# Optimization experiments

Hardware: AMD Instinct MI355X
Metric: run time of the kernel (lower is better)

## Reference

```python
import jax, jax.numpy as jnp
import numpy as np
import math

DIM = 256; SEQ = 2048; BSZ = 32; NI = 128; NS = 4; ITERS = 3

def _ln(x, g, b):
    m = x.mean(-1, keepdims=True)
    v = ((x - m) ** 2).mean(-1, keepdims=True)
    return (x - m) / jnp.sqrt(v + 1e-5) * g + b

def _norm(x):
    # torch F.normalize: x / ||x||.clamp_min(1e-12)
    return x / jnp.clip(jnp.linalg.norm(x, axis=-1, keepdims=True), 1e-12, None)

def setup_inputs() -> dict:
    key = jax.random.key(0)
    ks = jax.random.split(key, 16)
    def w(k, shape, s=0.02):
        return jax.random.normal(k, shape, jnp.float32) * s
    return {
        'tokens': jax.random.normal(ks[0], (BSZ, SEQ, DIM), jnp.float32),
        'cls_embed': jax.random.normal(ks[1], (BSZ, DIM), jnp.float32),
        'intent_queries': jax.random.normal(ks[2], (NI, DIM), jnp.float32),
        'noise': jax.random.normal(ks[3], (NI, BSZ, NS, DIM), jnp.float32),
        'Wk': w(ks[4], (DIM, DIM)), 'bk': jnp.zeros(DIM, jnp.float32),
        'Wv': w(ks[5], (DIM, DIM)), 'bv': jnp.zeros(DIM, jnp.float32),
        'Wqs': w(ks[6], (DIM, DIM)), 'bqs': jnp.zeros(DIM, jnp.float32),
        'Wqi': w(ks[7], (DIM, DIM)), 'bqi': jnp.zeros(DIM, jnp.float32),
        'ln1_g': jnp.ones(DIM, jnp.float32), 'ln1_b': jnp.zeros(DIM, jnp.float32),
        'ln2_g': jnp.ones(DIM, jnp.float32), 'ln2_b': jnp.zeros(DIM, jnp.float32),
        'Wf1': w(ks[8], (DIM, 2 * DIM)), 'bf1': jnp.zeros(2 * DIM, jnp.float32),
        'Wf2': w(ks[9], (2 * DIM, DIM)), 'bf2': jnp.zeros(DIM, jnp.float32),
        'slot_mu': w(ks[10], (1, NS, DIM)),  # randn*0.02
        'slot_sigma': jnp.ones((1, NS, DIM), jnp.float32) * 0.1,
        'alpha': jnp.float32(1.0),
        'temperature': jnp.float32(1.0),
    }

def reference(tokens, cls_embed, intent_queries, noise, Wk, bk, Wv, bv,
              Wqs, bqs, Wqi, bqi, ln1_g, ln1_b, ln2_g, ln2_b,
              Wf1, bf1, Wf2, bf2, slot_mu, slot_sigma, alpha, temperature):
    scale = 1.0 / math.sqrt(DIM)
    # k/v are identical across the per-intent loop in the original -> compute once
    k = tokens @ Wk + bk  # [B,S,D]
    v = tokens @ Wv + bv  # [B,S,D]
    cls_n = _norm(cls_embed)  # [B,D]

    def per_intent(q, eps):  # q: [D], eps: [B,NS,D]
        qn = _norm(q)
        q_intent = (q @ Wqi + bqi)[None, None, :]  # broadcast over [B,NS,:]
        slots = slot_mu[0] + eps * slot_sigma[0]   # [B,NS,D]
        for _ in range(ITERS):
            q_slot = slots @ Wqs + bqs + q_intent
            logit = jnp.einsum('bnd,bsd->bns', q_slot, k) * scale
            attn = jax.nn.softmax(logit, axis=-1)
            upd = jnp.einsum('bns,bsd->bnd', attn, v)
            slots = _ln(slots + upd, ln1_g, ln1_b)
            h = _ln(slots, ln2_g, ln2_b)
            slots = slots + jax.nn.gelu(h @ Wf1 + bf1, approximate=False) @ Wf2 + bf2
        sn = _norm(slots)                               # [B,NS,D]
        a = jax.nn.softmax(jnp.einsum('bnd,d->bn', sn, qn), axis=-1)
        summ = jnp.einsum('bn,bnd->bd', a, slots)       # slot_summary
        fused = cls_n + alpha * _norm(summ)
        return fused @ qn                               # [B]

    scores = jax.vmap(per_intent)(intent_queries, noise)  # [NI,B]
    logits = scores.T / jnp.maximum(temperature, 1e-4)    # [B,NI]
    return logits
```

## Files before the change

### kernel.cpp

```cpp
#include <hip/hip_runtime.h>
#include <math.h>

#define BSZ 32
#define NI  128

typedef __attribute__((ext_vector_type(8))) _Float16 f16x8;
typedef __attribute__((ext_vector_type(4))) _Float16 f16x4;
typedef __attribute__((ext_vector_type(4))) float    f32x4;

#define MFMA16(a, b, c) __builtin_amdgcn_mfma_f32_16x16x32_f16((a), (b), (c), 0, 0, 0)

#define GLL(g, l) __builtin_amdgcn_global_load_lds(                          \
    (const __attribute__((address_space(1))) void*)(g),                      \
    (__attribute__((address_space(3))) void*)(l), 16, 0, 0)

#define LGKM_BAR() do {                                                      \
    asm volatile("s_waitcnt lgkmcnt(0)" ::: "memory");                       \
    __builtin_amdgcn_sched_barrier(0);                                       \
    __builtin_amdgcn_s_barrier();                                            \
    __builtin_amdgcn_sched_barrier(0); } while (0)

__device__ inline float dot4f(float4 a, float4 b) {
    return a.x * b.x + a.y * b.y + a.z * b.z + a.w * b.w;
}

__device__ inline float4* slp(float* base, int r, int c) {
    return (float4*)(base + r * 256 + ((((c) >> 2) ^ (r & 7)) << 2));
}

__device__ inline void tpose64(const float* __restrict__ src, int Csrc,
                               _Float16* __restrict__ dstT, int KT,
                               int r0, int c0, _Float16 (*tbuf)[72], int tid)
{
#pragma unroll
    for (int it = 0; it < 4; it++) {
        int idx = tid + it * 256;
        int rr = idx >> 4, c4 = idx & 15;
        float4 w = *(const float4*)(src + (size_t)(r0 + rr) * Csrc + c0 + c4 * 4);
        tbuf[c4 * 4 + 0][rr] = (_Float16)w.x;
        tbuf[c4 * 4 + 1][rr] = (_Float16)w.y;
        tbuf[c4 * 4 + 2][rr] = (_Float16)w.z;
        tbuf[c4 * 4 + 3][rr] = (_Float16)w.w;
    }
    __syncthreads();
#pragma unroll
    for (int it = 0; it < 2; it++) {
        int idx = tid + it * 256;
        int orr = idx >> 3, oc8 = idx & 7;
        int n = c0 + orr;
        size_t tile = (size_t)(n >> 4) * KT + (r0 >> 5) + (oc8 >> 2);
        *(f16x8*)(dstT + tile * 512 + (n & 15) * 32 + (oc8 & 3) * 8) = *(const f16x8*)&tbuf[orr][oc8 * 8];
    }
}

__global__ __launch_bounds__(256) void prep(
    const float* __restrict__ Wk, const float* __restrict__ Wv,
    const float* __restrict__ Wqs, const float* __restrict__ Wf1,
    const float* __restrict__ Wf2,
    const float* __restrict__ intent_q, const float* __restrict__ Wqi,
    const float* __restrict__ bqi, const float* __restrict__ bqs,
    const float* __restrict__ cls_embed,
    _Float16* __restrict__ wkT, _Float16* __restrict__ wvT,
    _Float16* __restrict__ wqsT, _Float16* __restrict__ wf1T,
    _Float16* __restrict__ wf2T,
    float* __restrict__ qint2, float* __restrict__ qn, float* __restrict__ clsn)
{
    __shared__ _Float16 tbuf[64][72];
    __shared__ float buf[256];
    __shared__ float red[4];
    const int t = threadIdx.x, blk = blockIdx.x;
    const int lane = t & 63, w = t >> 6;

    if (blk < 112) {
        if (blk < 16)       tpose64(Wk, 256, wkT, 8, (blk >> 2) * 64, (blk & 3) * 64, tbuf, t);
        else if (blk < 32)  { int tt = blk - 16; tpose64(Wv, 256, wvT, 8, (tt >> 2) * 64, (tt & 3) * 64, tbuf, t); }
        else if (blk < 48)  { int tt = blk - 32; tpose64(Wqs, 256, wqsT, 8, (tt >> 2) * 64, (tt & 3) * 64, tbuf, t); }
        else if (blk < 80)  { int tt = blk - 48; tpose64(Wf1, 512, wf1T, 8, (tt & 3) * 64, (tt >> 2) * 64, tbuf, t); }
        else                { int tt = blk - 80; tpose64(Wf2, 256, wf2T, 16, (tt >> 2) * 64, (tt & 3) * 64, tbuf, t); }
    } else if (blk < 240) {
        int i = blk - 112;
        float x = intent_q[(size_t)i * 256 + t];
        buf[t] = x;
        float ss = x * x;
#pragma unroll
        for (int m = 1; m < 64; m <<= 1) ss += __shfl_xor(ss, m, 64);
        if (lane == 0) red[w] = ss;
        __syncthreads();
        float tot = red[0] + red[1] + red[2] + red[3];
        qn[(size_t)i * 256 + t] = x / fmaxf(sqrtf(tot), 1e-12f);
        float acc = bqi[t] + bqs[t];
        for (int e = 0; e < 256; e += 4) {
            const float4 q4 = *(const float4*)&buf[e];
            acc += q4.x * Wqi[(size_t)(e + 0) * 256 + t];
            acc += q4.y * Wqi[(size_t)(e + 1) * 256 + t];
            acc += q4.z * Wqi[(size_t)(e + 2) * 256 + t];
            acc += q4.w * Wqi[(size_t)(e + 3) * 256 + t];
        }
        qint2[(size_t)i * 256 + t] = acc;
    } else {
        int b = blk - 240;
        float x = cls_embed[(size_t)b * 256 + t];
        float ss = x * x;
#pragma unroll
        for (int m = 1; m < 64; m <<= 1) ss += __shfl_xor(ss, m, 64);
        if (lane == 0) red[w] = ss;
        __syncthreads();
        float tot = red[0] + red[1] + red[2] + red[3];
        clsn[(size_t)b * 256 + t] = x / fmaxf(sqrtf(tot), 1e-12f);
    }
}

__global__ __launch_bounds__(512, 2) void kvf_k(
    const float* __restrict__ tokens,
    const _Float16* __restrict__ wkT, const _Float16* __restrict__ wvT,
    const float* __restrict__ bk, const float* __restrict__ bv,
    _Float16* __restrict__ kT, _Float16* __restrict__ vT)
{
    __shared__ __align__(16) _Float16 Sb[2][8192];

    const int t = threadIdx.x, lane = t & 63, w = t >> 6;
    const int l15 = lane & 15, quad = lane >> 4;
    const int lofs = l15 * 32 + quad * 8;
    const int bx = blockIdx.x;
    const int b = bx & 31, chunk = bx >> 5;

    f16x8 wk[2][8], wv[2][8];
#pragma unroll
    for (int j = 0; j < 2; j++)
#pragma unroll
        for (int ks = 0; ks < 8; ks++) {
            wk[j][ks] = *(const f16x8*)(wkT + ((size_t)(2 * w + j) * 8 + ks) * 512 + lofs);
            wv[j][ks] = *(const f16x8*)(wvT + ((size_t)(2 * w + j) * 8 + ks) * 512 + lofs);
        }
    f32x4 bi0 = *(const f32x4*)(bk + w * 32 + quad * 4);
    f32x4 bi1 = *(const f32x4*)(bk + w * 32 + 16 + quad * 4);
    const float bv0 = bv[(2 * w) * 16 + l15];
    const float bv1 = bv[(2 * w + 1) * 16 + l15];

    const int rr = t >> 5, d8 = t & 31;
    const float* tbase = tokens + ((size_t)b * 2048 + chunk * 256) * 256 + rr * 256 + d8 * 8;
    const int wofs0 = (d8 >> 2) * 512 + rr * 32 + (d8 & 3) * 8;
    const int wofs1 = (8 + (d8 >> 2)) * 512 + rr * 32 + (d8 & 3) * 8;

    float4 pa0, pa1, pb0, pb1;

#define KVF_LOADS(P) do {                                                    \
        const float* sp_ = tbase + (size_t)(P) * 8192;                       \
        pa0 = *(const float4*)(sp_);                                         \
        pa1 = *(const float4*)(sp_ + 4);                                     \
        pb0 = *(const float4*)(sp_ + 4096);                                  \
        pb1 = *(const float4*)(sp_ + 4100);                                  \
    } while (0)

#define KVF_STAGE(BUF) do {                                                  \
        f16x8 h0, h1;                                                        \
        h0[0] = (_Float16)pa0.x; h0[1] = (_Float16)pa0.y;                    \
        h0[2] = (_Float16)pa0.z; h0[3] = (_Float16)pa0.w;                    \
        h0[4] = (_Float16)pa1.x; h0[5] = (_Float16)pa1.y;                    \
        h0[6] = (_Float16)pa1.z; h0[7] = (_Float16)pa1.w;                    \
        h1[0] = (_Float16)pb0.x; h1[1] = (_Float16)pb0.y;                    \
        h1[2] = (_Float16)pb0.z; h1[3] = (_Float16)pb0.w;                    \
        h1[4] = (_Float16)pb1.x; h1[5] = (_Float16)pb1.y;                    \
        h1[6] = (_Float16)pb1.z; h1[7] = (_Float16)pb1.w;                    \
        *(f16x8*)((BUF) + wofs0) = h0;                                       \
        *(f16x8*)((BUF) + wofs1) = h1;                                       \
    } while (0)

    KVF_LOADS(0);
    KVF_STAGE(&Sb[0][0]);
    LGKM_BAR();

    for (int p = 0; p < 8; p++) {
        if (p < 7) KVF_LOADS(p + 1);
        __builtin_amdgcn_sched_barrier(0);

        const _Float16* lb = &Sb[p & 1][0];
        const int stg0 = chunk * 16 + p * 2;
        const int sp = chunk * 8 + p;

        f16x8 a[2][8];
#pragma unroll
        for (int st = 0; st < 2; st++)
#pragma unroll
            for (int ks = 0; ks < 8; ks++)
                a[st][ks] = *(const f16x8*)(lb + (st * 8 + ks) * 512 + lofs);

#pragma unroll
        for (int st = 0; st < 2; st++) {
            f32x4 c0 = {0.f, 0.f, 0.f, 0.f}, c1 = {0.f, 0.f, 0.f, 0.f};
#pragma unroll
            for (int ks = 0; ks < 8; ks++) {
                c0 = MFMA16(wk[0][ks], a[st][ks], c0);
                c1 = MFMA16(wk[1][ks], a[st][ks], c1);
            }
            f16x4 p0, p1;
#pragma unroll
            for (int reg = 0; reg < 4; reg++) {
                p0[reg] = (_Float16)(c0[reg] + bi0[reg]);
                p1[reg] = (_Float16)(c1[reg] + bi1[reg]);
            }
            _Float16* tp = kT + ((size_t)(b * 128 + stg0 + st) * 8 + w) * 512 + l15 * 32;
            *(f16x4*)(tp + (quad >> 1) * 8 + (quad & 1) * 4) = p0;
            *(f16x4*)(tp + (2 + (quad >> 1)) * 8 + (quad & 1) * 4) = p1;
        }

#pragma unroll
        for (int j = 0; j < 2; j++) {
            f32x4 c0 = {0.f, 0.f, 0.f, 0.f}, c1 = {0.f, 0.f, 0.f, 0.f};
#pragma unroll
            for (int ks = 0; ks < 8; ks++) {
                c0 = MFMA16(a[0][ks], wv[j][ks], c0);
                c1 = MFMA16(a[1][ks], wv[j][ks], c1);
            }
            const float bb = j ? bv1 : bv0;
            f16x4 p0, p1;
#pragma unroll
            for (int reg = 0; reg < 4; reg++) {
                p0[reg] = (_Float16)(c0[reg] + bb);
                p1[reg] = (_Float16)(c1[reg] + bb);
            }
            _Float16* tp = vT + ((size_t)(b * 16 + 2 * w + j) * 64 + sp) * 512 + l15 * 32;
            *(f16x4*)(tp + (quad >> 1) * 8 + (quad & 1) * 4) = p0;
            *(f16x4*)(tp + (2 + (quad >> 1)) * 8 + (quad & 1) * 4) = p1;
        }

        if (p < 7) {
            KVF_STAGE(&Sb[(p + 1) & 1][0]);
            LGKM_BAR();
        }
    }
#undef KVF_LOADS
#undef KVF_STAGE
}

__global__ __launch_bounds__(256) void slots_init(
    const float* __restrict__ noise, const float* __restrict__ slot_mu,
    const float* __restrict__ slot_sigma, float* __restrict__ slots,
    _Float16* __restrict__ slotsT)
{
    int idx = blockIdx.x * 256 + threadIdx.x;
    int row = idx >> 5, d8 = idx & 31;
    int b = row >> 9, i = (row >> 2) & 127, n = row & 3;
    int d = d8 * 8;
    const float* mp = slot_mu + n * 256 + d;
    const float* sp = slot_sigma + n * 256 + d;
    const float* np = noise + (((size_t)i * BSZ + b) * 4 + n) * 256 + d;
    float4 o0, o1;
    {
        float4 mu = *(const float4*)mp, sg = *(const float4*)sp, ns = *(const float4*)np;
        o0.x = mu.x + ns.x * sg.x; o0.y = mu.y + ns.y * sg.y;
        o0.z = mu.z + ns.z * sg.z; o0.w = mu.w + ns.w * sg.w;
    }
    {
        float4 mu = *(const float4*)(mp + 4), sg = *(const float4*)(sp + 4), ns = *(const float4*)(np + 4);
        o1.x = mu.x + ns.x * sg.x; o1.y = mu.y + ns.y * sg.y;
        o1.z = mu.z + ns.z * sg.z; o1.w = mu.w + ns.w * sg.w;
    }
    *(float4*)(slots + (size_t)row * 256 + d) = o0;
    *(float4*)(slots + (size_t)row * 256 + d + 4) = o1;
    f16x8 h;
    h[0] = (_Float16)o0.x; h[1] = (_Float16)o0.y; h[2] = (_Float16)o0.z; h[3] = (_Float16)o0.w;
    h[4] = (_Float16)o1.x; h[5] = (_Float16)o1.y; h[6] = (_Float16)o1.z; h[7] = (_Float16)o1.w;
    *(f16x8*)(slotsT + ((size_t)(row >> 4) * 8 + (d8 >> 2)) * 512 + (row & 15) * 32 + (d8 & 3) * 8) = h;
}

__global__ __launch_bounds__(256) void qslot_k(
    const _Float16* __restrict__ slotsT, const _Float16* __restrict__ wqsT,
    const float* __restrict__ qint2, _Float16* __restrict__ qsT)
{
    const int tid = threadIdx.x, lane = tid & 63, wv = tid >> 6;
    const int l15 = lane & 15, quad = lane >> 4;
    const int lofs = l15 * 32 + quad * 8;
    const int bx = blockIdx.x, rb = bx >> 2, dq = bx & 3;
    const int rt = rb * 4 + wv;
    const int gr0 = rt * 16;

    f16x8 bs[8];
#pragma unroll
    for (int ks = 0; ks < 8; ks++)
        bs[ks] = *(const f16x8*)(slotsT + ((size_t)rt * 8 + ks) * 512 + lofs);
    const int iq = ((gr0 + l15) & 511) >> 2;
#pragma unroll
    for (int dt = 0; dt < 4; dt++) {
        int dti = dq * 4 + dt;
        f32x4 c = {0.f, 0.f, 0.f, 0.f};
#pragma unroll
        for (int ks = 0; ks < 8; ks++)
            c = MFMA16(*(const f16x8*)(wqsT + ((size_t)dti * 8 + ks) * 512 + lofs), bs[ks], c);
        float4 qi = *(const float4*)(qint2 + (size_t)iq * 256 + dti * 16 + quad * 4);
        f16x4 o;
#pragma unroll
        for (int reg = 0; reg < 4; reg++) o[reg] = (_Float16)((c[reg] + qi[reg]) * 0.0625f);
        *(f16x4*)(qsT + ((size_t)rt * 8 + (dti >> 1)) * 512 + l15 * 32
                  + ((dti & 1) * 2 + (quad >> 1)) * 8 + (quad & 1) * 4) = o;
    }
}

__global__ __launch_bounds__(512, 2) void attn_k(
    const _Float16* __restrict__ qsT, const _Float16* __restrict__ kT,
    const _Float16* __restrict__ vT,
    _Float16* __restrict__ Opart, float* __restrict__ psum4)
{
    __shared__ __align__(16) _Float16 Kb[2][16384];
    __shared__ __align__(16) _Float16 Vb[16384];
    __shared__ __align__(16) _Float16 pb[8][2304];

    const int tid = threadIdx.x, lane = tid & 63, wv = tid >> 6;
    const int l15 = lane & 15, quad = lane >> 4;
    const int lofs = l15 * 32 + quad * 8;
    const int bx = blockIdx.x;
    const int b = bx & 31, rb = (bx >> 5) & 1, sk = bx >> 6;
    const int gr0 = b * 512 + rb * 256 + wv * 32;
    const int rt_q = gr0 >> 4;

    _Float16* pw = pb[wv];

    const _Float16* kSrc = kT + ((size_t)(b * 128 + sk * 32) * 8) * 512;

    {
        const _Float16* src = kSrc + (size_t)(wv * 4) * 512 + lane * 8;
        _Float16* dst = &Kb[0][(wv * 4) * 512 + lane * 8];
#pragma unroll
        for (int j = 0; j < 4; j++) GLL(src + j * 512, dst + j * 512);
    }

    f16x8 q[2][8];
#pragma unroll
    for (int m = 0; m < 2; m++)
#pragma unroll
        for (int ks = 0; ks < 8; ks++)
            q[m][ks] = *(const f16x8*)(qsT + ((size_t)(rt_q + m) * 8 + ks) * 512 + lofs);

    f32x4 O[2][16];
#pragma unroll
    for (int m = 0; m < 2; m++)
#pragma unroll
        for (int dt = 0; dt < 16; dt++) O[m][dt] = (f32x4){0.f, 0.f, 0.f, 0.f};
    float ps[2][4] = {{0.f, 0.f, 0.f, 0.f}, {0.f, 0.f, 0.f, 0.f}};

    asm volatile("s_waitcnt vmcnt(0)" ::: "memory");
    __builtin_amdgcn_s_barrier();
    __builtin_amdgcn_sched_barrier(0);

    for (int s = 0; s < 8; s++) {
        const int cur = s & 1;

        {
            const int seg0 = wv * 4;
#pragma unroll
            for (int j = 0; j < 4; j++) {
                const int seg = seg0 + j;
                const _Float16* src = vT
                    + ((size_t)(b * 16 + (seg >> 1)) * 64 + sk * 16 + s * 2 + (seg & 1)) * 512
                    + lane * 8;
                GLL(src, &Vb[seg * 512 + lane * 8]);
            }
        }
        if (s < 7) {
            const _Float16* src = kSrc + (size_t)(s + 1) * 16384 + (wv * 4) * 512 + lane * 8;
            _Float16* dst = &Kb[cur ^ 1][(wv * 4) * 512 + lane * 8];
#pragma unroll
            for (int j = 0; j < 4; j++) GLL(src + j * 512, dst + j * 512);
            asm volatile("s_waitcnt vmcnt(8)" ::: "memory");
        } else {
            asm volatile("s_waitcnt vmcnt(4)" ::: "memory");
        }
        __builtin_amdgcn_s_barrier();
        __builtin_amdgcn_sched_barrier(0);

#pragma unroll
        for (int kt = 0; kt < 4; kt++) {
            const _Float16* kp = &Kb[cur][(kt * 8) * 512 + lofs];
            f32x4 c0 = {0.f, 0.f, 0.f, 0.f}, c1 = {0.f, 0.f, 0.f, 0.f};
#pragma unroll
            for (int ks = 0; ks < 8; ks++) {
                f16x8 kf = *(const f16x8*)(kp + ks * 512);
                c0 = MFMA16(q[0][ks], kf, c0);
                c1 = MFMA16(q[1][ks], kf, c1);
            }
            const int col = kt * 16 + l15;
#pragma unroll
            for (int reg = 0; reg < 4; reg++) {
                float p0 = __expf(fminf(c0[reg], 10.5f));
                float p1 = __expf(fminf(c1[reg], 10.5f));
                ps[0][reg] += p0;
                ps[1][reg] += p1;
                pw[(quad * 4 + reg) * 72 + col] = (_Float16)p0;
                pw[(16 + quad * 4 + reg) * 72 + col] = (_Float16)p1;
            }
        }

        __builtin_amdgcn_sched_barrier(0);
        if (s < 7) {
            asm volatile("s_waitcnt vmcnt(4)" ::: "memory");
        } else {
            asm volatile("s_waitcnt vmcnt(0)" ::: "memory");
        }
        __builtin_amdgcn_s_barrier();
        __builtin_amdgcn_sched_barrier(0);

        f16x8 pa[2][2];
#pragma unroll
        for (int m = 0; m < 2; m++)
#pragma unroll
            for (int kg = 0; kg < 2; kg++)
                pa[m][kg] = *(const f16x8*)(pw + (m * 16 + l15) * 72 + kg * 32 + quad * 8);
#pragma unroll
        for (int dt = 0; dt < 16; dt++) {
            const _Float16* vp = &Vb[dt * 1024 + lofs];
            f16x8 v0 = *(const f16x8*)(vp);
            f16x8 v1 = *(const f16x8*)(vp + 512);
            O[0][dt] = MFMA16(pa[0][0], v0, O[0][dt]);
            O[0][dt] = MFMA16(pa[0][1], v1, O[0][dt]);
            O[1][dt] = MFMA16(pa[1][0], v0, O[1][dt]);
            O[1][dt] = MFMA16(pa[1][1], v1, O[1][dt]);
        }

        __builtin_amdgcn_sched_barrier(0);
        __builtin_amdgcn_s_barrier();
        __builtin_amdgcn_sched_barrier(0);
    }

#pragma unroll
    for (int m = 0; m < 2; m++) {
#pragma unroll
        for (int msk = 1; msk <= 8; msk <<= 1)
#pragma unroll
            for (int reg = 0; reg < 4; reg++) ps[m][reg] += __shfl_xor(ps[m][reg], msk, 64);
        if (l15 == 0) {
#pragma unroll
            for (int reg = 0; reg < 4; reg++)
                psum4[(size_t)sk * 16384 + gr0 + m * 16 + quad * 4 + reg] = ps[m][reg];
        }
    }

#pragma unroll
    for (int m = 0; m < 2; m++) {
#pragma unroll
        for (int hd = 0; hd < 2; hd++) {
#pragma unroll
            for (int dt = 0; dt < 8; dt++) {
                const int dti = hd * 8 + dt;
#pragma unroll
                for (int reg = 0; reg < 4; reg++)
                    pw[(quad * 4 + reg) * 136 + dt * 16 + l15] = (_Float16)O[m][dti][reg];
            }
#pragma unroll
            for (int p2 = 0; p2 < 4; p2++) {
                const int u = lane + p2 * 64;
                const int row = u >> 4, col8 = u & 15;
                *(f16x8*)(Opart + ((size_t)sk * 16384 + gr0 + m * 16 + row) * 256 + hd * 128 + col8 * 8) =
                    *(const f16x8*)(pw + row * 136 + col8 * 8);
            }
        }
    }
}

__global__ __launch_bounds__(512, 1) void mlp_k(
    const _Float16* __restrict__ Opart, const float* __restrict__ psum4,
    float* __restrict__ slots,
    const float* __restrict__ ln1_g, const float* __restrict__ ln1_b,
    const float* __restrict__ ln2_g, const float* __restrict__ ln2_b,
    const _Float16* __restrict__ wf1T, const float* __restrict__ bf1,
    const _Float16* __restrict__ wf2T, const float* __restrict__ bf2,
    const _Float16* __restrict__ wqsT, const float* __restrict__ qint2,
    _Float16* __restrict__ qsT,
    const float* __restrict__ qn, const float* __restrict__ clsn,
    const float* __restrict__ alphap, const float* __restrict__ tempp,
    float* __restrict__ out, int it)
{
    __shared__ float sl[64 * 256];
    __shared__ float2 st2[64];
    __shared__ __align__(16) _Float16 actL[32768];

    const int tid = threadIdx.x, lane = tid & 63, w8 = tid >> 6;
    const int l15 = lane & 15, quad = lane >> 4;
    const int lofs = l15 * 32 + quad * 8;
    const int pairW = w8 >> 1, half = w8 & 1;
    const int bx = blockIdx.x;
    const int b = bx & 31, rg = bx >> 5;
    const int R0 = b * 512 + rg * 64;

#pragma unroll
    for (int r2 = 0; r2 < 2; r2++) {
        const int lr = w8 * 8 + r2 * 4 + quad;
        const int gr = R0 + lr;
        float l = 0.f;
#pragma unroll
        for (int j = 0; j < 4; j++) l += psum4[(size_t)j * 16384 + gr];
        const float invl = 1.f / l;
        float4 y[4];
        float sm = 0.f, sq = 0.f;
#pragma unroll
        for (int k = 0; k < 4; k++) {
            const int c = k * 64 + l15 * 4;
            float4 o4 = {0.f, 0.f, 0.f, 0.f};
#pragma unroll
            for (int j = 0; j < 4; j++) {
                f16x4 p = *(const f16x4*)(Opart + ((size_t)j * 16384 + gr) * 256 + c);
                o4.x += (float)p[0]; o4.y += (float)p[1];
                o4.z += (float)p[2]; o4.w += (float)p[3];
            }
            float4 s4 = *(const float4*)(slots + (size_t)gr * 256 + c);
            y[k].x = s4.x + o4.x * invl; y[k].y = s4.y + o4.y * invl;
            y[k].z = s4.z + o4.z * invl; y[k].w = s4.w + o4.w * invl;
            sm += y[k].x + y[k].y + y[k].z + y[k].w;
            sq += dot4f(y[k], y[k]);
        }
#pragma unroll
        for (int m = 1; m <= 8; m <<= 1) { sm += __shfl_xor(sm, m, 64); sq += __shfl_xor(sq, m, 64); }
        const float mean = sm * (1.f / 256.f);
        const float rstd = rsqrtf(sq * (1.f / 256.f) - mean * mean + 1e-5f);
        float sm2 = 0.f, sq2 = 0.f;
#pragma unroll
        for (int k = 0; k < 4; k++) {
            const int c = k * 64 + l15 * 4;
            float4 g1 = *(const float4*)(ln1_g + c);
            float4 b1 = *(const float4*)(ln1_b + c);
            float4 x1;
            x1.x = (y[k].x - mean) * rstd * g1.x + b1.x;
            x1.y = (y[k].y - mean) * rstd * g1.y + b1.y;
            x1.z = (y[k].z - mean) * rstd * g1.z + b1.z;
            x1.w = (y[k].w - mean) * rstd * g1.w + b1.w;
            *slp(sl, lr, c) = x1;
            sm2 += x1.x + x1.y + x1.z + x1.w;
            sq2 += dot4f(x1, x1);
        }
#pragma unroll
        for (int m = 1; m <= 8; m <<= 1) { sm2 += __shfl_xor(sm2, m, 64); sq2 += __shfl_xor(sq2, m, 64); }
        const float mean2 = sm2 * (1.f / 256.f);
        const float rstd2 = rsqrtf(sq2 * (1.f / 256.f) - mean2 * mean2 + 1e-5f);
        if (l15 == 0) st2[lr] = make_float2(mean2, rstd2);
    }
    __syncthreads();

    const int lrf = pairW * 16 + l15;
    {
        const float2 s2 = st2[lrf];
        f16x8 bh[8];
#pragma unroll
        for (int ks = 0; ks < 8; ks++) {
            const int c0 = ks * 32 + quad * 8;
            float4 xa = *slp(sl, lrf, c0);
            float4 xb = *slp(sl, lrf, c0 + 4);
            float4 ga = *(const float4*)(ln2_g + c0);
            float4 gb = *(const float4*)(ln2_g + c0 + 4);
            float4 ba = *(const float4*)(ln2_b + c0);
            float4 bb2 = *(const float4*)(ln2_b + c0 + 4);
            bh[ks][0] = (_Float16)((xa.x - s2.x) * s2.y * ga.x + ba.x);
            bh[ks][1] = (_Float16)((xa.y - s2.x) * s2.y * ga.y + ba.y);
            bh[ks][2] = (_Float16)((xa.z - s2.x) * s2.y * ga.z + ba.z);
            bh[ks][3] = (_Float16)((xa.w - s2.x) * s2.y * ga.w + ba.w);
            bh[ks][4] = (_Float16)((xb.x - s2.x) * s2.y * gb.x + bb2.x);
            bh[ks][5] = (_Float16)((xb.y - s2.x) * s2.y * gb.y + bb2.y);
            bh[ks][6] = (_Float16)((xb.z - s2.x) * s2.y * gb.z + bb2.z);
            bh[ks][7] = (_Float16)((xb.w - s2.x) * s2.y * gb.w + bb2.w);
        }
#pragma unroll 2
        for (int t16 = 0; t16 < 16; t16++) {
            const int hti = half * 16 + t16;
            f32x4 c = {0.f, 0.f, 0.f, 0.f};
#pragma unroll
            for (int ks = 0; ks < 8; ks++)
                c = MFMA16(*(const f16x8*)(wf1T + ((size_t)hti * 8 + ks) * 512 + lofs), bh[ks], c);
            float4 bb = *(const float4*)(bf1 + hti * 16 + quad * 4);
            f16x4 o;
#pragma unroll
            for (int reg = 0; reg < 4; reg++) {
                float xg = c[reg] + bb[reg];
                o[reg] = (_Float16)(0.5f * xg * (1.f + erff(xg * 0.70710678118654752f)));
            }
            *(f16x4*)(actL + ((size_t)(pairW * 16 + (hti >> 1))) * 512 + l15 * 32
                      + ((hti & 1) * 2 + (quad >> 1)) * 8 + (quad & 1) * 4) = o;
        }
    }
    __syncthreads();

    {
        f32x4 c[8];
#pragma unroll
        for (int d = 0; d < 8; d++) {
            const int dti = half * 8 + d;
            float4 x4 = *slp(sl, lrf, dti * 16 + quad * 4);
            float4 bb = *(const float4*)(bf2 + dti * 16 + quad * 4);
            c[d] = (f32x4){x4.x + bb.x, x4.y + bb.y, x4.z + bb.z, x4.w + bb.w};
        }
        const _Float16* ap = actL + ((size_t)pairW * 16) * 512 + lofs;
        for (int ks = 0; ks < 16; ks++) {
            f16x8 afrag = *(const f16x8*)(ap + (size_t)ks * 512);
#pragma unroll
            for (int d = 0; d < 8; d++)
                c[d] = MFMA16(*(const f16x8*)(wf2T + ((size_t)(half * 8 + d) * 16 + ks) * 512 + lofs),
                              afrag, c[d]);
        }
#pragma unroll
        for (int d = 0; d < 8; d++) {
            const int dti = half * 8 + d;
            float4 v = {c[d][0], c[d][1], c[d][2], c[d][3]};
            *slp(sl, lrf, dti * 16 + quad * 4) = v;
        }
    }
    __syncthreads();

    if (it < 2) {
        f16x8 bs[8];
#pragma unroll
        for (int ks = 0; ks < 8; ks++) {
            const int c0 = ks * 32 + quad * 8;
            float4 xa = *slp(sl, lrf, c0);
            float4 xb = *slp(sl, lrf, c0 + 4);
            bs[ks][0] = (_Float16)xa.x; bs[ks][1] = (_Float16)xa.y;
            bs[ks][2] = (_Float16)xa.z; bs[ks][3] = (_Float16)xa.w;
            bs[ks][4] = (_Float16)xb.x; bs[ks][5] = (_Float16)xb.y;
            bs[ks][6] = (_Float16)xb.z; bs[ks][7] = (_Float16)xb.w;
        }
        const int iq = (rg * 64 + pairW * 16 + l15) >> 2;
        const int rtg = b * 32 + rg * 4 + pairW;
#pragma unroll
        for (int d = 0; d < 8; d++) {
            const int dti = half * 8 + d;
            f32x4 c = {0.f, 0.f, 0.f, 0.f};
#pragma unroll
            for (int ks = 0; ks < 8; ks++)
                c = MFMA16(*(const f16x8*)(wqsT + ((size_t)dti * 8 + ks) * 512 + lofs), bs[ks], c);
            float4 qi = *(const float4*)(qint2 + (size_t)iq * 256 + dti * 16 + quad * 4);
            f16x4 o;
#pragma unroll
            for (int reg = 0; reg < 4; reg++) o[reg] = (_Float16)((c[reg] + qi[reg]) * 0.0625f);
            *(f16x4*)(qsT + ((size_t)rtg * 8 + (dti >> 1)) * 512 + l15 * 32
                      + ((dti & 1) * 2 + (quad >> 1)) * 8 + (quad & 1) * 4) = o;
        }
        {
            const int lr2 = tid >> 3, k8 = tid & 7;
#pragma unroll
            for (int q4 = 0; q4 < 8; q4++) {
                float4 v = *slp(sl, lr2, k8 * 32 + q4 * 4);
                *(float4*)(slots + (size_t)(R0 + lr2) * 256 + k8 * 32 + q4 * 4) = v;
            }
        }
    } else {
#pragma unroll
        for (int ii = 0; ii < 2; ii++) {
            const int i_loc = w8 * 2 + ii;
            const int i = rg * 16 + i_loc;
            float4 qv = *(const float4*)(qn + (size_t)i * 256 + lane * 4);
            float4 xs[4];
            float st4[4];
#pragma unroll
            for (int n = 0; n < 4; n++) {
                xs[n] = *slp(sl, i_loc * 4 + n, lane * 4);
                float ss = dot4f(xs[n], xs[n]);
                float sq = dot4f(xs[n], qv);
#pragma unroll
                for (int m = 1; m < 64; m <<= 1) { ss += __shfl_xor(ss, m, 64); sq += __shfl_xor(sq, m, 64); }
                st4[n] = sq / fmaxf(sqrtf(ss), 1e-12f);
            }
            float mx = fmaxf(fmaxf(st4[0], st4[1]), fmaxf(st4[2], st4[3]));
            float e0 = __expf(st4[0] - mx), e1 = __expf(st4[1] - mx);
            float e2 = __expf(st4[2] - mx), e3 = __expf(st4[3] - mx);
            float inv = 1.f / (e0 + e1 + e2 + e3);
            float4 smv;
            smv.x = (e0 * xs[0].x + e1 * xs[1].x + e2 * xs[2].x + e3 * xs[3].x) * inv;
            smv.y = (e0 * xs[0].y + e1 * xs[1].y + e2 * xs[2].y + e3 * xs[3].y) * inv;
            smv.z = (e0 * xs[0].z + e1 * xs[1].z + e2 * xs[2].z + e3 * xs[3].z) * inv;
            smv.w = (e0 * xs[0].w + e1 * xs[1].w + e2 * xs[2].w + e3 * xs[3].w) * inv;
            float ssm = dot4f(smv, smv);
            float sqn = dot4f(smv, qv);
            float4 cv = *(const float4*)(clsn + (size_t)b * 256 + lane * 4);
            float cq = dot4f(cv, qv);
#pragma unroll
            for (int m = 1; m < 64; m <<= 1) {
                ssm += __shfl_xor(ssm, m, 64);
                sqn += __shfl_xor(sqn, m, 64);
                cq  += __shfl_xor(cq,  m, 64);
            }
            if (lane == 0) {
                float score = cq + alphap[0] * sqn / fmaxf(sqrtf(ssm), 1e-12f);
                out[(size_t)b * NI + i] = score / fmaxf(tempp[0], 1e-4f);
            }
        }
    }
}

extern "C" void kernel_launch(void* const* d_in, const int* in_sizes, int n_in,
                              void* d_out, int out_size, void* d_ws, size_t ws_size,
                              hipStream_t stream)
{
    const float* tokens     = (const float*)d_in[0];
    const float* cls_embed  = (const float*)d_in[1];
    const float* intent_q   = (const float*)d_in[2];
    const float* noise      = (const float*)d_in[3];
    const float* Wk  = (const float*)d_in[4];
    const float* bk  = (const float*)d_in[5];
    const float* Wv  = (const float*)d_in[6];
    const float* bv  = (const float*)d_in[7];
    const float* Wqs = (const float*)d_in[8];
    const float* bqs = (const float*)d_in[9];
    const float* Wqi = (const float*)d_in[10];
    const float* bqi = (const float*)d_in[11];
    const float* ln1g = (const float*)d_in[12];
    const float* ln1b = (const float*)d_in[13];
    const float* ln2g = (const float*)d_in[14];
    const float* ln2b = (const float*)d_in[15];
    const float* Wf1 = (const float*)d_in[16];
    const float* bf1 = (const float*)d_in[17];
    const float* Wf2 = (const float*)d_in[18];
    const float* bf2 = (const float*)d_in[19];
    const float* slot_mu    = (const float*)d_in[20];
    const float* slot_sigma = (const float*)d_in[21];
    const float* alphap = (const float*)d_in[22];
    const float* tempp  = (const float*)d_in[23];
    float* out = (float*)d_out;

    char* base = (char*)d_ws;
    _Float16* qsT   = (_Float16*)(base);
    _Float16* slotsT= (_Float16*)(base + 8388608u);
    _Float16* kT    = (_Float16*)(base + 33554432u);
    _Float16* vT    = (_Float16*)(base + 67108864u);
    _Float16* Opart = (_Float16*)(base + 100663296u);
    float* slots    = (float*)(base + 134217728u);
    _Float16* wkT   = (_Float16*)(base + 150994944u);
    _Float16* wvT   = (_Float16*)(base + 151126016u);
    _Float16* wqsT  = (_Float16*)(base + 151257088u);
    _Float16* wf1T  = (_Float16*)(base + 151388160u);
    _Float16* wf2T  = (_Float16*)(base + 151650304u);
    float* qint2    = (float*)(base + 151912448u);
    float* qnb      = (float*)(base + 152043520u);
    float* clsn     = (float*)(base + 152174592u);
    float* psum4    = (float*)(base + 152207360u);

    prep<<<272, 256, 0, stream>>>(Wk, Wv, Wqs, Wf1, Wf2, intent_q, Wqi, bqi, bqs,
                                  cls_embed, wkT, wvT, wqsT, wf1T, wf2T,
                                  qint2, qnb, clsn);
    kvf_k<<<256, 512, 0, stream>>>(tokens, wkT, wvT, bk, bv, kT, vT);
    slots_init<<<2048, 256, 0, stream>>>(noise, slot_mu, slot_sigma, slots, slotsT);
    qslot_k<<<1024, 256, 0, stream>>>(slotsT, wqsT, qint2, qsT);

    for (int it = 0; it < 3; it++) {
        attn_k<<<256, 512, 0, stream>>>(qsT, kT, vT, Opart, psum4);
        mlp_k<<<256, 512, 0, stream>>>(Opart, psum4, slots,
                                       ln1g, ln1b, ln2g, ln2b,
                                       wf1T, bf1, wf2T, bf2,
                                       wqsT, qint2, qsT,
                                       qnb, clsn, alphap, tempp, out, it);
    }
}
```

Measured before the change: 499.2 us.

## Swizzle LDS fragment layouts and halve mlp_k block size

Adds an XOR swizzle to the LDS layouts of the token tile in kvf_k, the K/V tiles in attn_k (applied through the global-to-LDS source addresses) and the GELU activations in mlp_k. The goal is to cut LDS bank conflicts on the MFMA fragment reads. Separately, mlp_k is split into 512 blocks of 256 threads covering 32 rows each, with a two-blocks-per-CU launch bound, to raise occupancy and parallelism. The swizzle depends on matching index math across producers and consumers, and any mismatch would give wrong results.

```diff
diff --git a/kernel.cpp b/kernel.cpp
--- a/kernel.cpp
+++ b/kernel.cpp
@@ -121,6 +121,7 @@
     const int t = threadIdx.x, lane = t & 63, w = t >> 6;
     const int l15 = lane & 15, quad = lane >> 4;
     const int lofs = l15 * 32 + quad * 8;
+    const int lofsA = ((l15 * 4 + quad) ^ ((l15 >> 1) & 7)) * 8;
     const int bx = blockIdx.x;
     const int b = bx & 31, chunk = bx >> 5;
 
@@ -139,8 +140,9 @@
 
     const int rr = t >> 5, d8 = t & 31;
     const float* tbase = tokens + ((size_t)b * 2048 + chunk * 256) * 256 + rr * 256 + d8 * 8;
-    const int wofs0 = (d8 >> 2) * 512 + rr * 32 + (d8 & 3) * 8;
-    const int wofs1 = (8 + (d8 >> 2)) * 512 + rr * 32 + (d8 & 3) * 8;
+    const int mskW = ((rr >> 1) & 7) ^ (((d8 >> 2) & 3) << 1);
+    const int wofs0 = (d8 >> 2) * 512 + (((rr * 4 + (d8 & 3)) ^ mskW) * 8);
+    const int wofs1 = wofs0 + 8 * 512;
 
     float4 pa0, pa1, pb0, pb1;
 
@@ -183,7 +185,7 @@
         for (int st = 0; st < 2; st++)
 #pragma unroll
             for (int ks = 0; ks < 8; ks++)
-                a[st][ks] = *(const f16x8*)(lb + (st * 8 + ks) * 512 + lofs);
+                a[st][ks] = *(const f16x8*)(lb + (st * 8 + ks) * 512 + (lofsA ^ ((ks & 3) * 16)));
 
 #pragma unroll
         for (int st = 0; st < 2; st++) {
@@ -308,6 +310,8 @@
     const int tid = threadIdx.x, lane = tid & 63, wv = tid >> 6;
     const int l15 = lane & 15, quad = lane >> 4;
     const int lofs = l15 * 32 + quad * 8;
+    const int lofsA = ((l15 * 4 + quad) ^ ((l15 >> 1) & 7)) * 8;
+    const int lnsw = (lane ^ ((lane >> 3) & 7)) * 8;
     const int bx = blockIdx.x;
     const int b = bx & 31, rb = (bx >> 5) & 1, sk = bx >> 6;
     const int gr0 = b * 512 + rb * 256 + wv * 32;
@@ -318,7 +322,7 @@
     const _Float16* kSrc = kT + ((size_t)(b * 128 + sk * 32) * 8) * 512;
 
     {
-        const _Float16* src = kSrc + (size_t)(wv * 4) * 512 + lane * 8;
+        const _Float16* src = kSrc + (size_t)(wv * 4) * 512 + lnsw;
         _Float16* dst = &Kb[0][(wv * 4) * 512 + lane * 8];
 #pragma unroll
         for (int j = 0; j < 4; j++) GLL(src + j * 512, dst + j * 512);
@@ -352,12 +356,12 @@
                 const int seg = seg0 + j;
                 const _Float16* src = vT
                     + ((size_t)(b * 16 + (seg >> 1)) * 64 + sk * 16 + s * 2 + (seg & 1)) * 512
-                    + lane * 8;
+                    + lnsw;
                 GLL(src, &Vb[seg * 512 + lane * 8]);
             }
         }
         if (s < 7) {
-            const _Float16* src = kSrc + (size_t)(s + 1) * 16384 + (wv * 4) * 512 + lane * 8;
+            const _Float16* src = kSrc + (size_t)(s + 1) * 16384 + (wv * 4) * 512 + lnsw;
             _Float16* dst = &Kb[cur ^ 1][(wv * 4) * 512 + lane * 8];
 #pragma unroll
             for (int j = 0; j < 4; j++) GLL(src + j * 512, dst + j * 512);
@@ -370,11 +374,11 @@
 
 #pragma unroll
         for (int kt = 0; kt < 4; kt++) {
-            const _Float16* kp = &Kb[cur][(kt * 8) * 512 + lofs];
+            const _Float16* kp = &Kb[cur][(kt * 8) * 512];
             f32x4 c0 = {0.f, 0.f, 0.f, 0.f}, c1 = {0.f, 0.f, 0.f, 0.f};
 #pragma unroll
             for (int ks = 0; ks < 8; ks++) {
-                f16x8 kf = *(const f16x8*)(kp + ks * 512);
+                f16x8 kf = *(const f16x8*)(kp + ks * 512 + lofsA);
                 c0 = MFMA16(q[0][ks], kf, c0);
                 c1 = MFMA16(q[1][ks], kf, c1);
             }
@@ -407,9 +411,9 @@
                 pa[m][kg] = *(const f16x8*)(pw + (m * 16 + l15) * 72 + kg * 32 + quad * 8);
 #pragma unroll
         for (int dt = 0; dt < 16; dt++) {
-            const _Float16* vp = &Vb[dt * 1024 + lofs];
-            f16x8 v0 = *(const f16x8*)(vp);
-            f16x8 v1 = *(const f16x8*)(vp + 512);
+            const _Float16* vp = &Vb[dt * 1024];
+            f16x8 v0 = *(const f16x8*)(vp + lofsA);
+            f16x8 v1 = *(const f16x8*)(vp + 512 + lofsA);
             O[0][dt] = MFMA16(pa[0][0], v0, O[0][dt]);
             O[0][dt] = MFMA16(pa[0][1], v1, O[0][dt]);
             O[1][dt] = MFMA16(pa[1][0], v0, O[1][dt]);
@@ -456,7 +460,7 @@
     }
 }
 
-__global__ __launch_bounds__(512, 1) void mlp_k(
+__global__ __launch_bounds__(256, 2) void mlp_k(
     const _Float16* __restrict__ Opart, const float* __restrict__ psum4,
     float* __restrict__ slots,
     const float* __restrict__ ln1_g, const float* __restrict__ ln1_b,
@@ -469,21 +473,22 @@
     const float* __restrict__ alphap, const float* __restrict__ tempp,
     float* __restrict__ out, int it)
 {
-    __shared__ float sl[64 * 256];
-    __shared__ float2 st2[64];
-    __shared__ __align__(16) _Float16 actL[32768];
-
-    const int tid = threadIdx.x, lane = tid & 63, w8 = tid >> 6;
+    __shared__ float sl[32 * 256];
+    __shared__ float2 st2[32];
+    __shared__ __align__(16) _Float16 actL[16384];
+
+    const int tid = threadIdx.x, lane = tid & 63, w4 = tid >> 6;
     const int l15 = lane & 15, quad = lane >> 4;
     const int lofs = l15 * 32 + quad * 8;
-    const int pairW = w8 >> 1, half = w8 & 1;
+    const int lofsA = ((l15 * 4 + quad) ^ ((l15 >> 1) & 7)) * 8;
+    const int pairW = w4 >> 1, half = w4 & 1;
     const int bx = blockIdx.x;
     const int b = bx & 31, rg = bx >> 5;
-    const int R0 = b * 512 + rg * 64;
+    const int R0 = b * 512 + rg * 32;
 
 #pragma unroll
     for (int r2 = 0; r2 < 2; r2++) {
-        const int lr = w8 * 8 + r2 * 4 + quad;
+        const int lr = w4 * 8 + r2 * 4 + quad;
         const int gr = R0 + lr;
         float l = 0.f;
 #pragma unroll
@@ -570,8 +575,9 @@
                 float xg = c[reg] + bb[reg];
                 o[reg] = (_Float16)(0.5f * xg * (1.f + erff(xg * 0.70710678118654752f)));
             }
-            *(f16x4*)(actL + ((size_t)(pairW * 16 + (hti >> 1))) * 512 + l15 * 32
-                      + ((hti & 1) * 2 + (quad >> 1)) * 8 + (quad & 1) * 4) = o;
+            const int gA = l15 * 4 + (hti & 1) * 2 + (quad >> 1);
+            *(f16x4*)(actL + ((size_t)(pairW * 16 + (hti >> 1))) * 512
+                      + ((gA ^ ((l15 >> 1) & 7)) * 8) + (quad & 1) * 4) = o;
         }
     }
     __syncthreads();
@@ -585,9 +591,9 @@
             float4 bb = *(const float4*)(bf2 + dti * 16 + quad * 4);
             c[d] = (f32x4){x4.x + bb.x, x4.y + bb.y, x4.z + bb.z, x4.w + bb.w};
         }
-        const _Float16* ap = actL + ((size_t)pairW * 16) * 512 + lofs;
+        const _Float16* ap = actL + ((size_t)pairW * 16) * 512;
         for (int ks = 0; ks < 16; ks++) {
-            f16x8 afrag = *(const f16x8*)(ap + (size_t)ks * 512);
+            f16x8 afrag = *(const f16x8*)(ap + (size_t)ks * 512 + lofsA);
 #pragma unroll
             for (int d = 0; d < 8; d++)
                 c[d] = MFMA16(*(const f16x8*)(wf2T + ((size_t)(half * 8 + d) * 16 + ks) * 512 + lofs),
@@ -614,8 +620,8 @@
             bs[ks][4] = (_Float16)xb.x; bs[ks][5] = (_Float16)xb.y;
             bs[ks][6] = (_Float16)xb.z; bs[ks][7] = (_Float16)xb.w;
         }
-        const int iq = (rg * 64 + pairW * 16 + l15) >> 2;
-        const int rtg = b * 32 + rg * 4 + pairW;
+        const int iq = (rg * 32 + pairW * 16 + l15) >> 2;
+        const int rtg = b * 32 + rg * 2 + pairW;
 #pragma unroll
         for (int d = 0; d < 8; d++) {
             const int dti = half * 8 + d;
@@ -641,8 +647,8 @@
     } else {
 #pragma unroll
         for (int ii = 0; ii < 2; ii++) {
-            const int i_loc = w8 * 2 + ii;
-            const int i = rg * 16 + i_loc;
+            const int i_loc = w4 * 2 + ii;
+            const int i = rg * 8 + i_loc;
             float4 qv = *(const float4*)(qn + (size_t)i * 256 + lane * 4);
             float4 xs[4];
             float st4[4];
@@ -738,7 +744,7 @@
 
     for (int it = 0; it < 3; it++) {
         attn_k<<<256, 512, 0, stream>>>(qsT, kT, vT, Opart, psum4);
-        mlp_k<<<256, 512, 0, stream>>>(Opart, psum4, slots,
+        mlp_k<<<512, 256, 0, stream>>>(Opart, psum4, slots,
                                        ln1g, ln1b, ln2g, ln2b,
                                        wf1T, bf1, wf2T, bf2,
                                        wqsT, qint2, qsT,
```

New measurement: 490.0 us. Within noise of the previous version (-1.9%).
